# Performance work log

Measured on AMD Instinct MI355X. Metric: run time of the kernel, lower is better.

Reference implementation:

```python
import jax, jax.numpy as jnp
import numpy as np

# res_scale = (max(scale)+float_scale)/max(scale) = 2.5/2 = 1.25
RES_SCALE = 1.25


def _dct(x):
    # DCT-II via FFT (Makhoul), norm=None, matching torch module's dct().
    # x: [..., N]
    N = x.shape[-1]
    v = jnp.concatenate([x[..., ::2], x[..., 1::2][..., ::-1]], axis=-1)
    Vc = jnp.fft.fft(v, axis=-1)  # full FFT == _rfft(onesided=False)
    k = -jnp.arange(N, dtype=x.dtype) * (np.pi / (2.0 * N))
    V = 2.0 * (Vc.real * jnp.cos(k) - Vc.imag * jnp.sin(k))
    return V.astype(x.dtype)


def _idct(X):
    # Inverse of DCT-II (norm=None), matching torch module's idct().
    # X: [..., N]
    N = X.shape[-1]
    Xv = X / 2.0
    k = jnp.arange(N, dtype=X.dtype) * (np.pi / (2.0 * N))
    Wr, Wi = jnp.cos(k), jnp.sin(k)
    Vt_r = Xv
    Vt_i = jnp.concatenate([jnp.zeros_like(Xv[..., :1]), -Xv[..., ::-1][..., :-1]], axis=-1)
    V_r = Vt_r * Wr - Vt_i * Wi
    V_i = Vt_r * Wi + Vt_i * Wr
    # _irfft(onesided=False): keep first N//2+1 bins, irfft back to length N
    Vc = (V_r[..., : N // 2 + 1] + 1j * V_i[..., : N // 2 + 1]).astype(jnp.complex64)
    v = jnp.fft.irfft(Vc, n=N, axis=-1).astype(X.dtype)
    # odd/even de-shuffle
    x = jnp.zeros_like(v)
    x = x.at[..., ::2].set(v[..., : N - N // 2])
    x = x.at[..., 1::2].set(v[..., ::-1][..., : N // 2])
    return x


def _dct_2d(x):
    return jnp.swapaxes(_dct(jnp.swapaxes(_dct(x), -1, -2)), -1, -2)


def _idct_2d(X):
    return jnp.swapaxes(_idct(jnp.swapaxes(_idct(X), -1, -2)), -1, -2)


def setup_inputs() -> dict:
    key = jax.random.key(0)
    x = jax.random.normal(key, (16, 3, 768, 768), dtype=jnp.float32)
    return {"x": x}


def reference(x):
    B, C, H, W = x.shape
    outH, outW = int(H * RES_SCALE), int(W * RES_SCALE)
    X = _dct_2d(x)
    # ZeroPad2d((0, outW-W, 0, outH-H)): pad right and bottom with zeros
    X = jnp.pad(X, ((0, 0), (0, 0), (0, outH - H), (0, outW - W)))
    return _idct_2d(X)
```

## Files before the change

kernel.cpp:

```cpp
#include <hip/hip_runtime.h>


#define HW 768
#define OHW 960
#define NIMG 48

typedef __attribute__((ext_vector_type(8))) short short8;
typedef __attribute__((ext_vector_type(4))) float f32x4;

__device__ __forceinline__ unsigned short f2bf(float f) {
    union { float f; unsigned int u; } v; v.f = f;
    unsigned int u = v.u;
    return (unsigned short)((u + 0x7FFFu + ((u >> 16) & 1u)) >> 16);
}

__device__ __forceinline__ void glds16(const void* g, void* l) {
    __builtin_amdgcn_global_load_lds(
        (const __attribute__((address_space(1))) void*)g,
        (__attribute__((address_space(3))) void*)l, 16, 0, 0);
}

__device__ __forceinline__ float dsum(int p) {
    int n1 = (767 * p) % 30720;
    int n2 = (768 * p) % 30720;
    const float w = (float)(3.14159265358979323846 / 15360.0);
    float s1 = sinf((float)n1 * w);
    float c2 = cosf((float)n2 * w);
    float s3 = sinf((float)p * w);
    return s1 * c2 / s3;
}

__global__ void fill_M(unsigned short* __restrict__ Mb) {
    int idx = blockIdx.x * 256 + threadIdx.x;
    if (idx >= OHW * HW) return;
    int i = idx / HW, n = idx - i * HW;
    int a = 8 * i + 4, b = 10 * n + 5;
    int p1 = a + b;
    int p2 = a - b; if (p2 < 0) p2 += 15360;
    float m = (1.0f + dsum(p1) + dsum(p2)) * (1.0f / 960.0f);
    Mb[idx] = f2bf(m);
}

__global__ void transpose_conv(const float* __restrict__ x, unsigned short* __restrict__ xT) {
    __shared__ float tile[32][33];
    int img = blockIdx.z;
    int h0 = blockIdx.y * 32, w0 = blockIdx.x * 32;
    const float* xi = x + (size_t)img * HW * HW;
    unsigned short* xo = xT + (size_t)img * HW * HW;
    int tx = threadIdx.x, ty = threadIdx.y;
#pragma unroll
    for (int r = 0; r < 4; ++r)
        tile[ty + 8 * r][tx] = xi[(size_t)(h0 + ty + 8 * r) * HW + (w0 + tx)];
    __syncthreads();
#pragma unroll
    for (int r = 0; r < 4; ++r)
        xo[(size_t)(w0 + ty + 8 * r) * HW + (h0 + tx)] = f2bf(tile[tx][ty + 8 * r]);
}

__global__ __launch_bounds__(256) void gemm_bt(
    const unsigned short* __restrict__ Ag, long long strideA, int lda,
    const unsigned short* __restrict__ Bg, long long strideB, int ldb,
    void* __restrict__ Cg, long long strideC, int ldc,
    int Md, int Nd, int Kd, int out_f32)
{
    __shared__ unsigned short As[128 * 32];
    __shared__ unsigned short Bs[128 * 32];

    const int tid = threadIdx.x;
    const int wave = tid >> 6, lane = tid & 63;
    const int wm = wave >> 1, wn = wave & 1;
    const int t16 = lane & 15, quad = lane >> 4;
    const int z = blockIdx.z;

    const unsigned short* A = Ag + (size_t)z * strideA;
    const unsigned short* B = Bg + (size_t)z * strideB;
    const int mb = blockIdx.y * 128, nbb = blockIdx.x * 128;

    f32x4 acc[4][4];
#pragma unroll
    for (int i = 0; i < 4; ++i)
#pragma unroll
        for (int j = 0; j < 4; ++j)
            acc[i][j] = (f32x4){0.f, 0.f, 0.f, 0.f};

    const int rowT = tid >> 2;
    const int kcT = (tid & 3) << 3;
    unsigned short* lA0 = As + wave * 512;
    unsigned short* lB0 = Bs + wave * 512;

    for (int k0 = 0; k0 < Kd; k0 += 32) {
#pragma unroll
        for (int it = 0; it < 2; ++it) {
            int row = rowT + it * 64;
            int gr = mb + row; if (gr >= Md) gr = Md - 1;
            glds16(A + (size_t)gr * lda + k0 + kcT, lA0 + it * 2048);
            int gn = nbb + row; if (gn >= Nd) gn = Nd - 1;
            glds16(B + (size_t)gn * ldb + k0 + kcT, lB0 + it * 2048);
        }
        __syncthreads();

        short8 af[4], bfr[4];
#pragma unroll
        for (int mi = 0; mi < 4; ++mi)
            af[mi] = *(const short8*)(&As[(wm * 64 + mi * 16 + t16) * 32 + quad * 8]);
#pragma unroll
        for (int ni = 0; ni < 4; ++ni)
            bfr[ni] = *(const short8*)(&Bs[(wn * 64 + ni * 16 + t16) * 32 + quad * 8]);
#pragma unroll
        for (int mi = 0; mi < 4; ++mi)
#pragma unroll
            for (int ni = 0; ni < 4; ++ni)
                acc[mi][ni] = __builtin_amdgcn_mfma_f32_16x16x32_bf16(
                    af[mi], bfr[ni], acc[mi][ni], 0, 0, 0);
        __syncthreads();
    }

    const int gr0 = mb + wm * 64;
    const int gc0 = nbb + wn * 64;
    if (out_f32) {
        float* C = (float*)Cg + (size_t)z * strideC;
#pragma unroll
        for (int mi = 0; mi < 4; ++mi)
#pragma unroll
            for (int ni = 0; ni < 4; ++ni) {
                int col = gc0 + ni * 16 + t16;
                if (col < Nd) {
#pragma unroll
                    for (int r = 0; r < 4; ++r) {
                        int rowg = gr0 + mi * 16 + quad * 4 + r;
                        if (rowg < Md) C[(size_t)rowg * ldc + col] = acc[mi][ni][r];
                    }
                }
            }
    } else {
        unsigned short* C = (unsigned short*)Cg + (size_t)z * strideC;
#pragma unroll
        for (int mi = 0; mi < 4; ++mi)
#pragma unroll
            for (int ni = 0; ni < 4; ++ni) {
                int col = gc0 + ni * 16 + t16;
                if (col < Nd) {
#pragma unroll
                    for (int r = 0; r < 4; ++r) {
                        int rowg = gr0 + mi * 16 + quad * 4 + r;
                        if (rowg < Md) C[(size_t)rowg * ldc + col] = f2bf(acc[mi][ni][r]);
                    }
                }
            }
    }
}

extern "C" void kernel_launch(void* const* d_in, const int* in_sizes, int n_in,
                              void* d_out, int out_size, void* d_ws, size_t ws_size,
                              hipStream_t stream) {
    const float* x = (const float*)d_in[0];
    float* out = (float*)d_out;
    char* ws = (char*)d_ws;

    size_t offM  = 0;
    size_t fixed = offM + (size_t)OHW * HW * 2;
    size_t perImg = (size_t)HW * HW * 2 + (size_t)OHW * HW * 2;

    int nb = 1;
    if (ws_size > fixed + perImg) {
        size_t q = (ws_size - fixed) / perImg;
        nb = (q > 48) ? 48 : (int)q;
        if (nb < 1) nb = 1;
    }

    unsigned short* Mb = (unsigned short*)(ws + offM);
    unsigned short* xT = (unsigned short*)(ws + fixed);
    unsigned short* T  = (unsigned short*)(ws + fixed + (size_t)nb * HW * HW * 2);

    fill_M<<<(OHW * HW + 255) / 256, 256, 0, stream>>>(Mb);

    for (int b0 = 0; b0 < NIMG; b0 += nb) {
        int cur = NIMG - b0; if (cur > nb) cur = nb;
        transpose_conv<<<dim3(24, 24, cur), dim3(32, 8), 0, stream>>>(
            x + (size_t)b0 * HW * HW, xT);
        gemm_bt<<<dim3(6, 8, cur), 256, 0, stream>>>(
            Mb, 0, HW, xT, (long long)HW * HW, HW,
            T, (long long)OHW * HW, HW, OHW, HW, HW, 0);
        gemm_bt<<<dim3(8, 8, cur), 256, 0, stream>>>(
            T, (long long)OHW * HW, HW, Mb, 0, HW,
            out + (size_t)b0 * OHW * OHW, (long long)OHW * OHW, OHW,
            OHW, OHW, HW, 1);
    }
    (void)in_sizes; (void)n_in; (void)out_size;
}
```

Before: 457.8 us.

## Drop the transpose pass by swapping GEMM operand order, and swizzle LDS tiles

Replaces the tiled transpose-and-convert kernel with a plain vectorized fp32-to-bf16 conversion. The first GEMM now produces (M·xᵀ)ᵀ and the second GEMM takes M as its A operand, so the final result is still M·x·Mᵀ without transposing the input. The GEMM's global-to-LDS loads permute the K chunks with an XOR swizzle, and the fragment reads use the matching XOR, to cut LDS bank conflicts. Per-iteration row clamping and address arithmetic are hoisted out of the K loop. The risk is that the swizzle and operand-order change must stay consistent for the output to be correct.

```diff
diff --git a/kernel.cpp b/kernel.cpp
--- a/kernel.cpp
+++ b/kernel.cpp
@@ -7,6 +7,8 @@
 
 typedef __attribute__((ext_vector_type(8))) short short8;
 typedef __attribute__((ext_vector_type(4))) float f32x4;
+typedef __attribute__((ext_vector_type(4))) float float4v;
+typedef __attribute__((ext_vector_type(4))) unsigned short us4;
 
 __device__ __forceinline__ unsigned short f2bf(float f) {
     union { float f; unsigned int u; } v; v.f = f;
@@ -24,10 +26,7 @@
     int n1 = (767 * p) % 30720;
     int n2 = (768 * p) % 30720;
     const float w = (float)(3.14159265358979323846 / 15360.0);
-    float s1 = sinf((float)n1 * w);
-    float c2 = cosf((float)n2 * w);
-    float s3 = sinf((float)p * w);
-    return s1 * c2 / s3;
+    return sinf((float)n1 * w) * cosf((float)n2 * w) / sinf((float)p * w);
 }
 
 __global__ void fill_M(unsigned short* __restrict__ Mb) {
@@ -41,24 +40,16 @@
     Mb[idx] = f2bf(m);
 }
 
-__global__ void transpose_conv(const float* __restrict__ x, unsigned short* __restrict__ xT) {
-    __shared__ float tile[32][33];
-    int img = blockIdx.z;
-    int h0 = blockIdx.y * 32, w0 = blockIdx.x * 32;
-    const float* xi = x + (size_t)img * HW * HW;
-    unsigned short* xo = xT + (size_t)img * HW * HW;
-    int tx = threadIdx.x, ty = threadIdx.y;
-#pragma unroll
-    for (int r = 0; r < 4; ++r)
-        tile[ty + 8 * r][tx] = xi[(size_t)(h0 + ty + 8 * r) * HW + (w0 + tx)];
-    __syncthreads();
-#pragma unroll
-    for (int r = 0; r < 4; ++r)
-        xo[(size_t)(w0 + ty + 8 * r) * HW + (h0 + tx)] = f2bf(tile[tx][ty + 8 * r]);
+__global__ void conv_bf16(const float* __restrict__ x, unsigned short* __restrict__ xb, int n4) {
+    int i = blockIdx.x * 256 + threadIdx.x;
+    if (i >= n4) return;
+    float4v v = *(const float4v*)(x + (size_t)i * 4);
+    us4 o; o.x = f2bf(v.x); o.y = f2bf(v.y); o.z = f2bf(v.z); o.w = f2bf(v.w);
+    *(us4*)(xb + (size_t)i * 4) = o;
 }
 
 __global__ __launch_bounds__(256) void gemm_bt(
-    const unsigned short* __restrict__ Ag, long long strideA, int lda,
+    const unsigned short* __restrict__ A, int lda,
     const unsigned short* __restrict__ Bg, long long strideB, int ldb,
     void* __restrict__ Cg, long long strideC, int ldc,
     int Md, int Nd, int Kd, int out_f32)
@@ -72,7 +63,6 @@
     const int t16 = lane & 15, quad = lane >> 4;
     const int z = blockIdx.z;
 
-    const unsigned short* A = Ag + (size_t)z * strideA;
     const unsigned short* B = Bg + (size_t)z * strideB;
     const int mb = blockIdx.y * 128, nbb = blockIdx.x * 128;
 
@@ -84,28 +74,37 @@
             acc[i][j] = (f32x4){0.f, 0.f, 0.f, 0.f};
 
     const int rowT = tid >> 2;
-    const int kcT = (tid & 3) << 3;
+    const int ksw = (((tid & 3) ^ ((rowT >> 1) & 3)) << 3);
     unsigned short* lA0 = As + wave * 512;
     unsigned short* lB0 = Bs + wave * 512;
 
+    int grA0 = mb + rowT;        if (grA0 >= Md) grA0 = Md - 1;
+    int grA1 = mb + rowT + 64;   if (grA1 >= Md) grA1 = Md - 1;
+    int gnB0 = nbb + rowT;       if (gnB0 >= Nd) gnB0 = Nd - 1;
+    int gnB1 = nbb + rowT + 64;  if (gnB1 >= Nd) gnB1 = Nd - 1;
+    const unsigned short* pA0 = A + (size_t)grA0 * lda + ksw;
+    const unsigned short* pA1 = A + (size_t)grA1 * lda + ksw;
+    const unsigned short* pB0 = B + (size_t)gnB0 * ldb + ksw;
+    const unsigned short* pB1 = B + (size_t)gnB1 * ldb + ksw;
+
+    const int quadx = quad ^ ((t16 >> 1) & 3);
+    const int aBase = (wm * 64 + t16) * 32 + quadx * 8;
+    const int bBase = (wn * 64 + t16) * 32 + quadx * 8;
+
     for (int k0 = 0; k0 < Kd; k0 += 32) {
-#pragma unroll
-        for (int it = 0; it < 2; ++it) {
-            int row = rowT + it * 64;
-            int gr = mb + row; if (gr >= Md) gr = Md - 1;
-            glds16(A + (size_t)gr * lda + k0 + kcT, lA0 + it * 2048);
-            int gn = nbb + row; if (gn >= Nd) gn = Nd - 1;
-            glds16(B + (size_t)gn * ldb + k0 + kcT, lB0 + it * 2048);
-        }
+        glds16(pA0 + k0, lA0);
+        glds16(pA1 + k0, lA0 + 2048);
+        glds16(pB0 + k0, lB0);
+        glds16(pB1 + k0, lB0 + 2048);
         __syncthreads();
 
         short8 af[4], bfr[4];
 #pragma unroll
         for (int mi = 0; mi < 4; ++mi)
-            af[mi] = *(const short8*)(&As[(wm * 64 + mi * 16 + t16) * 32 + quad * 8]);
+            af[mi] = *(const short8*)(&As[aBase + mi * 512]);
 #pragma unroll
         for (int ni = 0; ni < 4; ++ni)
-            bfr[ni] = *(const short8*)(&Bs[(wn * 64 + ni * 16 + t16) * 32 + quad * 8]);
+            bfr[ni] = *(const short8*)(&Bs[bBase + ni * 512]);
 #pragma unroll
         for (int mi = 0; mi < 4; ++mi)
 #pragma unroll
@@ -169,20 +168,21 @@
     }
 
     unsigned short* Mb = (unsigned short*)(ws + offM);
-    unsigned short* xT = (unsigned short*)(ws + fixed);
+    unsigned short* xb = (unsigned short*)(ws + fixed);
     unsigned short* T  = (unsigned short*)(ws + fixed + (size_t)nb * HW * HW * 2);
 
     fill_M<<<(OHW * HW + 255) / 256, 256, 0, stream>>>(Mb);
 
     for (int b0 = 0; b0 < NIMG; b0 += nb) {
         int cur = NIMG - b0; if (cur > nb) cur = nb;
-        transpose_conv<<<dim3(24, 24, cur), dim3(32, 8), 0, stream>>>(
-            x + (size_t)b0 * HW * HW, xT);
+        int n4 = cur * (HW * HW / 4);
+        conv_bf16<<<(n4 + 255) / 256, 256, 0, stream>>>(
+            x + (size_t)b0 * HW * HW, xb, n4);
         gemm_bt<<<dim3(6, 8, cur), 256, 0, stream>>>(
-            Mb, 0, HW, xT, (long long)HW * HW, HW,
+            Mb, HW, xb, (long long)HW * HW, HW,
             T, (long long)OHW * HW, HW, OHW, HW, HW, 0);
         gemm_bt<<<dim3(8, 8, cur), 256, 0, stream>>>(
-            T, (long long)OHW * HW, HW, Mb, 0, HW,
+            Mb, HW, T, (long long)OHW * HW, HW,
             out + (size_t)b0 * OHW * OHW, (long long)OHW * OHW, OHW,
             OHW, OHW, HW, 1);
     }
```

After: 428.6 us. 1.07x faster.
